# Kernel tuning notes

Measured on AMD Instinct MI355X. Metric: run time of the kernel, lower is better.

Reference implementation:

```python
import jax, jax.numpy as jnp
import numpy as np
import math

B, S, MEM, D, H = 2, 2048, 512, 1024, 16
DH = D // H  # 64


def setup_inputs() -> dict:
    key = jax.random.key(0)
    ks = jax.random.split(key, 12)
    s = 1.0 / math.sqrt(D)
    return {
        "x": jax.random.normal(ks[0], (B, S, D), jnp.float32),
        "mems": jax.random.normal(ks[1], (B, MEM, D), jnp.float32),
        "freqs_cis": jax.random.normal(ks[2], (S, 32), jnp.float32),
        "mask": jax.random.randint(ks[3], (B, MEM + S), 0, 2, jnp.int32),
        "Wq": jax.random.normal(ks[4], (D, D), jnp.float32) * s,
        "bq": jnp.zeros((D,), jnp.float32),
        "Wk": jax.random.normal(ks[5], (D, D), jnp.float32) * s,
        "bk": jnp.zeros((D,), jnp.float32),
        "Wv": jax.random.normal(ks[6], (D, D), jnp.float32) * s,
        "bv": jnp.zeros((D,), jnp.float32),
        "Wo": jax.random.normal(ks[7], (D, D), jnp.float32) * s,
        "bo": jnp.zeros((D,), jnp.float32),
    }


def _split_heads(t):
    # [B, T, D] -> [B, H, T, DH]
    b, t_, _ = t.shape
    return t.reshape(b, t_, H, DH).transpose(0, 2, 1, 3)


def reference(x, mems, freqs_cis, mask, Wq, bq, Wk, bk, Wv, bv, Wo, bo):
    # mems prepended along sequence for K/V (torch: c = cat([mems, x], 1))
    c = jnp.concatenate([mems, x], axis=1)  # [B, MEM+S, D]
    Q = _split_heads(x @ Wq.T + bq)          # [B, H, S, DH]
    K = _split_heads(c @ Wk.T + bk)          # [B, H, Skv, DH]
    V = _split_heads(c @ Wv.T + bv)          # [B, H, Skv, DH]

    scores = jnp.einsum("bhqd,bhkd->bhqk", Q, K) / math.sqrt(DH)
    m = mask.astype(jnp.float32)             # [B, Skv]
    scores = scores - 1e6 * (1.0 - m[:, None, None, :])
    attn = jax.nn.softmax(scores, axis=-1)   # dropout omitted (eval mode)
    out = jnp.einsum("bhqk,bhkd->bhqd", attn, V)  # [B, H, S, DH]
    out = out.transpose(0, 2, 1, 3).reshape(B, S, D)
    return out @ Wo.T + bo
```

## Files before the change

kernel.cpp:

```cpp
#include <hip/hip_runtime.h>
#include <math.h>

#define NB   2
#define SQ   2048
#define SMEM 512
#define SKVN 2560
#define ND   1024
#define NH   16
#define DHN  64

typedef unsigned short u16;
typedef short bf16x8 __attribute__((ext_vector_type(8)));
typedef float f32x4 __attribute__((ext_vector_type(4)));
typedef u16 u16x4 __attribute__((ext_vector_type(4)));
typedef u16 u16x8 __attribute__((ext_vector_type(8)));

#define CSC   0.1803368801111204f

__device__ __forceinline__ u16 f2bf(float f) {
    unsigned u = __float_as_uint(f);
    u += 0x7FFFu + ((u >> 16) & 1u);
    return (u16)(u >> 16);
}

__device__ __forceinline__ void async16(u16* lds, const u16* g) {
    __builtin_amdgcn_global_load_lds(
        (const __attribute__((address_space(1))) void*)g,
        (__attribute__((address_space(3))) void*)lds, 16, 0, 0);
}

__device__ __forceinline__ unsigned lds_off(const void* p) {
    return (unsigned)(uintptr_t)(const __attribute__((address_space(3))) void*)p;
}

__device__ __forceinline__ u16x4 tr_read(unsigned a) {
    u16x4 d;
    asm volatile("ds_read_b64_tr_b16 %0, %1" : "=v"(d) : "v"(a) : "memory");
    return d;
}

__device__ __forceinline__ unsigned cvtpk(float lo, float hi) {
    unsigned r;
    asm("v_cvt_pk_bf16_f32 %0, %1, %2" : "=v"(r) : "v"(lo), "v"(hi));
    return r;
}

__device__ __forceinline__ float exp2r(float x) {
    float r;
    asm("v_exp_f32 %0, %1" : "=v"(r) : "v"(x));
    return r;
}

union PKU { unsigned u[2]; u16x4 v; };
union U8  { struct { u16x4 lo, hi; } p; bf16x8 v; };

__global__ __launch_bounds__(256)
void cvt_all(const float* __restrict__ x, const float* __restrict__ mems,
             const float* __restrict__ W0, const float* __restrict__ W1,
             const float* __restrict__ W2, const float* __restrict__ W3,
             u16* __restrict__ xb, u16* __restrict__ memb,
             u16* __restrict__ d0, u16* __restrict__ d1,
             u16* __restrict__ d2, u16* __restrict__ d3,
             const int* __restrict__ mask, float* __restrict__ mbias)
{
    const int bid = blockIdx.x;
    if (bid >= 4608) {
        const int i = (bid - 4608) * 256 + threadIdx.x;
        if (i < NB * SKVN) mbias[i] = mask[i] ? 0.f : 1.0e6f * CSC;
        return;
    }
    size_t i = ((size_t)bid * 256 + threadIdx.x) * 8;
    const float* s; u16* d;
    if (i < 4194304) { s = x; d = xb; }
    else if (i < 5242880) { s = mems; d = memb; i -= 4194304; }
    else {
        size_t off = i - 5242880;
        const int wi = (int)(off >> 20);
        i = off & 1048575;
        switch (wi) {
            case 0:  s = W0; d = d0; break;
            case 1:  s = W1; d = d1; break;
            case 2:  s = W2; d = d2; break;
            default: s = W3; d = d3; break;
        }
    }
    float4 a = *(const float4*)(s + i);
    float4 b = *(const float4*)(s + i + 4);
    u16x8 o;
    o[0]=f2bf(a.x); o[1]=f2bf(a.y); o[2]=f2bf(a.z); o[3]=f2bf(a.w);
    o[4]=f2bf(b.x); o[5]=f2bf(b.y); o[6]=f2bf(b.z); o[7]=f2bf(b.w);
    *(u16x8*)(d + i) = o;
}

__device__ __forceinline__ const u16* arow_ptr(const u16* x, const u16* mems,
                                               int grow, int T, int memLen) {
    int b = grow >= T ? 1 : 0;
    int t = grow - b * T;
    if (memLen > 0 && t < memLen)
        return mems + ((size_t)(b * memLen + t)) * ND;
    return x + ((size_t)(b * (T - memLen) + (t - memLen))) * ND;
}

__device__ __forceinline__
void gemm_body(const u16* __restrict__ x, const u16* __restrict__ mems,
               const u16* __restrict__ W, const float* __restrict__ bias,
               void* __restrict__ out, int T, int memLen, int mode,
               int bx, int by, u16* As0, u16* As1, u16* Bs0, u16* Bs1)
{
    u16* As[2] = {As0, As1};
    u16* Bs[2] = {Bs0, Bs1};

    const int tid  = threadIdx.x;
    const int wave = tid >> 6, lane = tid & 63;
    const int lg = lane >> 4, li = lane & 15;
    const int wr = (wave >> 1) * 64, wc = (wave & 1) * 64;
    const int row0 = bx * 128, col0 = by * 128;

    const int srow = lane >> 2;
    const int sslot = lane & 3;

    f32x4 acc[4][4];
    const f32x4 zf = {0.f, 0.f, 0.f, 0.f};
#pragma unroll
    for (int m = 0; m < 4; ++m)
#pragma unroll
        for (int n = 0; n < 4; ++n) acc[m][n] = zf;

    auto stage = [&](int c, int kt) {
        const int k0 = kt * 32;
#pragma unroll
        for (int ch = wave; ch < 8; ch += 4) {
            const int r = ch * 16 + srow;
            const int gs = sslot ^ ((r ^ (r >> 2)) & 3);
            async16(&As[c][ch * 512],
                    arow_ptr(x, mems, row0 + r, T, memLen) + k0 + gs * 8);
        }
#pragma unroll
        for (int ch = wave; ch < 8; ch += 4) {
            const int r = ch * 16 + srow;
            const int gs = sslot ^ ((r ^ (r >> 2)) & 3);
            async16(&Bs[c][ch * 512],
                    W + (size_t)(col0 + r) * ND + k0 + gs * 8);
        }
    };

    stage(0, 0);
    int cur = 0;
    for (int kt = 0; kt < 32; ++kt) {
        __syncthreads();
        if (kt + 1 < 32) stage(cur ^ 1, kt + 1);

        bf16x8 af[4], bfr[4];
#pragma unroll
        for (int m = 0; m < 4; ++m) {
            const int r = wr + m * 16 + li;
            af[m] = *(const bf16x8*)&As[cur][r * 32 + ((lg ^ ((r ^ (r >> 2)) & 3)) << 3)];
        }
#pragma unroll
        for (int n = 0; n < 4; ++n) {
            const int r = wc + n * 16 + li;
            bfr[n] = *(const bf16x8*)&Bs[cur][r * 32 + ((lg ^ ((r ^ (r >> 2)) & 3)) << 3)];
        }
#pragma unroll
        for (int m = 0; m < 4; ++m)
#pragma unroll
            for (int n = 0; n < 4; ++n)
                acc[m][n] = __builtin_amdgcn_mfma_f32_16x16x32_bf16(
                                af[m], bfr[n], acc[m][n], 0, 0, 0);
        cur ^= 1;
    }

#pragma unroll
    for (int n = 0; n < 4; ++n) {
        const int col = col0 + wc + n * 16 + li;
        const float bv = bias[col];
#pragma unroll
        for (int m = 0; m < 4; ++m) {
            const int rbase = row0 + wr + m * 16 + 4 * lg;
            if (mode == 0) {
                float* o = (float*)out;
#pragma unroll
                for (int r = 0; r < 4; ++r)
                    o[(size_t)(rbase + r) * ND + col] = acc[m][n][r] + bv;
            } else if (mode == 1) {
                u16* o = (u16*)out;
                const int h = col >> 6, dh = col & 63;
#pragma unroll
                for (int r = 0; r < 4; ++r) {
                    const int grow = rbase + r;
                    const int b = grow >= T ? 1 : 0;
                    const int t = grow - b * T;
                    o[(((size_t)b * NH + h) * T + t) * DHN + dh] =
                        f2bf(acc[m][n][r] + bv);
                }
            } else {
                u16* o = (u16*)out;
                const int h = col >> 6, dh = col & 63;
                const int b = rbase >= T ? 1 : 0;
                const int t = rbase - b * T;
                u16x4 pk;
                pk[0] = f2bf(acc[m][n][0] + bv);
                pk[1] = f2bf(acc[m][n][1] + bv);
                pk[2] = f2bf(acc[m][n][2] + bv);
                pk[3] = f2bf(acc[m][n][3] + bv);
                *(u16x4*)&o[(((size_t)b * NH + h) * DHN + dh) * (size_t)T + t] = pk;
            }
        }
    }
}

__global__ __launch_bounds__(256)
void gemm_single(const u16* __restrict__ x, const u16* __restrict__ W,
                 const float* __restrict__ bias, void* __restrict__ out,
                 int T, int mode)
{
    __shared__ u16 As[2][128 * 32];
    __shared__ u16 Bs[2][128 * 32];
    gemm_body(x, nullptr, W, bias, out, T, 0, mode, blockIdx.x, blockIdx.y,
              As[0], As[1], Bs[0], Bs[1]);
}

__global__ __launch_bounds__(256)
void gemm_qkv(const u16* __restrict__ xb, const u16* __restrict__ memb,
              const u16* __restrict__ Wq, const float* __restrict__ bq, u16* Qb,
              const u16* __restrict__ Wk, const float* __restrict__ bk, u16* Kb,
              const u16* __restrict__ Wv, const float* __restrict__ bv, u16* Vtb)
{
    __shared__ u16 As[2][128 * 32];
    __shared__ u16 Bs[2][128 * 32];
    const int id = (blockIdx.x & 7) * 112 + (blockIdx.x >> 3);
    if (id < 256) {
        gemm_body(xb, nullptr, Wq, bq, Qb, SQ, 0, 1, id & 31, id >> 5,
                  As[0], As[1], Bs[0], Bs[1]);
    } else if (id < 576) {
        const int t = id - 256;
        gemm_body(xb, memb, Wk, bk, Kb, SKVN, SMEM, 1, t % 40, t / 40,
                  As[0], As[1], Bs[0], Bs[1]);
    } else {
        const int t = id - 576;
        gemm_body(xb, memb, Wv, bv, Vtb, SKVN, SMEM, 2, t % 40, t / 40,
                  As[0], As[1], Bs[0], Bs[1]);
    }
}

__global__ __launch_bounds__(256)
void attn_mfma(const u16* __restrict__ Qw, const u16* __restrict__ Kw,
               const u16* __restrict__ Vt, const float* __restrict__ mbias,
               u16* __restrict__ AO)
{
    __shared__ u16 Ks[2][64 * 64];
    __shared__ u16 Vs[2][64 * 64];
    __shared__ u16 Ps[4][2048];

    const int tid  = threadIdx.x;
    const int wave = tid >> 6, lane = tid & 63;
    const int lg = lane >> 4, li = lane & 15;

    const int wg = blockIdx.x;
    const int sw = (wg & 7) * 64 + (wg >> 3);
    const int bh = sw >> 4;
    const int q0 = (sw & 15) * 128;
    const int b = bh >> 4, h = bh & 15;

    const u16* Kg = Kw + (size_t)bh * SKVN * DHN;
    const u16* Vg = Vt + (size_t)bh * DHN * SKVN;
    const float* mrow = mbias + (size_t)b * SKVN;

    bf16x8 qA0, qA1, qB0, qB1;
    {
        const u16* Qp = Qw + ((size_t)bh * SQ + q0 + wave * 32 + li) * DHN;
        qA0 = *(const bf16x8*)(Qp + lg * 8);
        qA1 = *(const bf16x8*)(Qp + 32 + lg * 8);
        qB0 = *(const bf16x8*)(Qp + 16 * DHN + lg * 8);
        qB1 = *(const bf16x8*)(Qp + 16 * DHN + 32 + lg * 8);
    }

    U8 ou;
#pragma unroll
    for (int i = 0; i < 4; ++i) { ou.p.lo[i] = 0x3F80; ou.p.hi[i] = 0x3F80; }
    const bf16x8 onesb = ou.v;

    const int srow = lane >> 3, sslot = lane & 7;

    auto stage = [&](int c, int t) {
        const int kv0 = t * 64;
#pragma unroll
        for (int ch = wave; ch < 8; ch += 4) {
            const int r = ch * 8 + srow;
            async16(&Ks[c][ch * 512],
                    Kg + (size_t)(kv0 + r) * DHN + ((sslot ^ (r & 7)) << 3));
        }
#pragma unroll
        for (int ch = wave; ch < 8; ch += 4) {
            const int r = ch * 8 + srow;
            async16(&Vs[c][ch * 512],
                    Vg + (size_t)r * SKVN + kv0 + ((sslot ^ (r & 7)) << 3));
        }
    };

    f32x4 oA[4], oB[4], laccA, laccB;
    const f32x4 zf = {0.f, 0.f, 0.f, 0.f};
#pragma unroll
    for (int n = 0; n < 4; ++n) { oA[n] = zf; oB[n] = zf; }
    laccA = zf; laccB = zf;

    u16* Pw = &Ps[wave][0];
    const unsigned paA = lds_off(Pw) + 256u * lg + 8u * li;
    const unsigned paB = paA + 2048u;

    float mbn[4];
#pragma unroll
    for (int n = 0; n < 4; ++n) mbn[n] = mrow[n * 16 + li];

    stage(0, 0);
    int cur = 0;
    for (int t = 0; t < SKVN / 64; ++t) {
        float mbc[4];
#pragma unroll
        for (int n = 0; n < 4; ++n) mbc[n] = mbn[n];

        __syncthreads();
        if (t + 1 < SKVN / 64) {
            stage(cur ^ 1, t + 1);
#pragma unroll
            for (int n = 0; n < 4; ++n)
                mbn[n] = mrow[(t + 1) * 64 + n * 16 + li];
        }

        __builtin_amdgcn_s_setprio(1);
        f32x4 sA[4], sB[4];
#pragma unroll
        for (int n = 0; n < 4; ++n) {
            const int r = n * 16 + li;
            bf16x8 kb0 = *(const bf16x8*)&Ks[cur][r * 64 + ((lg ^ (r & 7)) << 3)];
            bf16x8 kb1 = *(const bf16x8*)&Ks[cur][r * 64 + (((4 + lg) ^ (r & 7)) << 3)];
            f32x4 z = zf;
            z     = __builtin_amdgcn_mfma_f32_16x16x32_bf16(qA0, kb0, z, 0, 0, 0);
            sA[n] = __builtin_amdgcn_mfma_f32_16x16x32_bf16(qA1, kb1, z, 0, 0, 0);
            f32x4 y = zf;
            y     = __builtin_amdgcn_mfma_f32_16x16x32_bf16(qB0, kb0, y, 0, 0, 0);
            sB[n] = __builtin_amdgcn_mfma_f32_16x16x32_bf16(qB1, kb1, y, 0, 0, 0);
        }
        __builtin_amdgcn_s_setprio(0);

#pragma unroll
        for (int n = 0; n < 4; ++n) {
            const float mb = mbc[n];
            const int pw = (n * 16 + li) * 16 + lg * 4;
            PKU ua;
            ua.u[0] = cvtpk(exp2r(fmaf(sA[n][0], CSC, -mb)),
                            exp2r(fmaf(sA[n][1], CSC, -mb)));
            ua.u[1] = cvtpk(exp2r(fmaf(sA[n][2], CSC, -mb)),
                            exp2r(fmaf(sA[n][3], CSC, -mb)));
            *(u16x4*)&Pw[pw] = ua.v;
            PKU ub;
            ub.u[0] = cvtpk(exp2r(fmaf(sB[n][0], CSC, -mb)),
                            exp2r(fmaf(sB[n][1], CSC, -mb)));
            ub.u[1] = cvtpk(exp2r(fmaf(sB[n][2], CSC, -mb)),
                            exp2r(fmaf(sB[n][3], CSC, -mb)));
            *(u16x4*)&Pw[1024 + pw] = ub.v;
        }

        u16x4 a00 = tr_read(paA);
        u16x4 a01 = tr_read(paA + 128);
        u16x4 a10 = tr_read(paA + 1024);
        u16x4 a11 = tr_read(paA + 1024 + 128);
        u16x4 b00 = tr_read(paB);
        u16x4 b01 = tr_read(paB + 128);
        u16x4 b10 = tr_read(paB + 1024);
        u16x4 b11 = tr_read(paB + 1024 + 128);
        asm volatile("s_waitcnt lgkmcnt(0)" ::: "memory");
        __builtin_amdgcn_sched_barrier(0);
        U8 pA0, pA1, pB0, pB1;
        pA0.p.lo = a00; pA0.p.hi = a01;
        pA1.p.lo = a10; pA1.p.hi = a11;
        pB0.p.lo = b00; pB0.p.hi = b01;
        pB1.p.lo = b10; pB1.p.hi = b11;

        __builtin_amdgcn_s_setprio(1);
        laccA = __builtin_amdgcn_mfma_f32_16x16x32_bf16(pA0.v, onesb, laccA, 0, 0, 0);
        laccA = __builtin_amdgcn_mfma_f32_16x16x32_bf16(pA1.v, onesb, laccA, 0, 0, 0);
        laccB = __builtin_amdgcn_mfma_f32_16x16x32_bf16(pB0.v, onesb, laccB, 0, 0, 0);
        laccB = __builtin_amdgcn_mfma_f32_16x16x32_bf16(pB1.v, onesb, laccB, 0, 0, 0);
#pragma unroll
        for (int n = 0; n < 4; ++n) {
            const int r = n * 16 + li;
            bf16x8 vb0 = *(const bf16x8*)&Vs[cur][r * 64 + ((lg ^ (r & 7)) << 3)];
            bf16x8 vb1 = *(const bf16x8*)&Vs[cur][r * 64 + (((4 + lg) ^ (r & 7)) << 3)];
            oA[n] = __builtin_amdgcn_mfma_f32_16x16x32_bf16(pA0.v, vb0, oA[n], 0, 0, 0);
            oA[n] = __builtin_amdgcn_mfma_f32_16x16x32_bf16(pA1.v, vb1, oA[n], 0, 0, 0);
            oB[n] = __builtin_amdgcn_mfma_f32_16x16x32_bf16(pB0.v, vb0, oB[n], 0, 0, 0);
            oB[n] = __builtin_amdgcn_mfma_f32_16x16x32_bf16(pB1.v, vb1, oB[n], 0, 0, 0);
        }
        __builtin_amdgcn_s_setprio(0);
        cur ^= 1;
    }

#pragma unroll
    for (int r = 0; r < 4; ++r) {
        const float invA = 1.f / laccA[r];
        const float invB = 1.f / laccB[r];
        const int rowA = q0 + wave * 32 + 4 * lg + r;
#pragma unroll
        for (int n = 0; n < 4; ++n) {
            const int col = h * DHN + n * 16 + li;
            AO[((size_t)b * SQ + rowA) * ND + col] = f2bf(oA[n][r] * invA);
            AO[((size_t)b * SQ + rowA + 16) * ND + col] = f2bf(oB[n][r] * invB);
        }
    }
}

extern "C" void kernel_launch(void* const* d_in, const int* in_sizes, int n_in,
                              void* d_out, int out_size, void* d_ws, size_t ws_size,
                              hipStream_t stream)
{
    const float* x    = (const float*)d_in[0];
    const float* mems = (const float*)d_in[1];
    const int*   mask = (const int*)d_in[3];
    const float* Wq = (const float*)d_in[4];  const float* bq = (const float*)d_in[5];
    const float* Wk = (const float*)d_in[6];  const float* bk = (const float*)d_in[7];
    const float* Wv = (const float*)d_in[8];  const float* bv = (const float*)d_in[9];
    const float* Wo = (const float*)d_in[10]; const float* bo = (const float*)d_in[11];
    float* out = (float*)d_out;

    u16* ws = (u16*)d_ws;
    u16* xb   = ws;
    u16* memb = xb   + (size_t)NB * SQ * ND;
    u16* Wqb  = memb + (size_t)NB * SMEM * ND;
    u16* Wkb  = Wqb + (size_t)ND * ND;
    u16* Wvb  = Wkb + (size_t)ND * ND;
    u16* Wob  = Wvb + (size_t)ND * ND;
    u16* Qb   = Wob + (size_t)ND * ND;
    u16* Kb   = Qb  + (size_t)NB * NH * SQ * DHN;
    u16* Vtb  = Kb  + (size_t)NB * NH * SKVN * DHN;
    u16* AOb  = Vtb + (size_t)NB * NH * SKVN * DHN;
    float* mbias = (float*)(AOb + (size_t)NB * SQ * ND);

    const dim3 blk(256);
    cvt_all<<<dim3(4628), blk, 0, stream>>>(x, mems, Wq, Wk, Wv, Wo,
                                            xb, memb, Wqb, Wkb, Wvb, Wob,
                                            mask, mbias);
    gemm_qkv<<<dim3(896), blk, 0, stream>>>(xb, memb,
                                            Wqb, bq, Qb,
                                            Wkb, bk, Kb,
                                            Wvb, bv, Vtb);
    attn_mfma<<<dim3(512), blk, 0, stream>>>(Qb, Kb, Vtb, mbias, AOb);
    gemm_single<<<dim3(32, 8), blk, 0, stream>>>(AOb, Wob, bo, (void*)out, SQ, 0);
}
```

Before: 172.8 us.

## Split attention KV range in two halves and add combine kernel

Result: slower. 177.5 us (+2.7%).

```diff
diff --git a/kernel.cpp b/kernel.cpp
--- a/kernel.cpp
+++ b/kernel.cpp
@@ -8,6 +8,7 @@
 #define ND   1024
 #define NH   16
 #define DHN  64
+#define NBH  32
 
 typedef unsigned short u16;
 typedef short bf16x8 __attribute__((ext_vector_type(8)));
@@ -21,6 +22,10 @@
     unsigned u = __float_as_uint(f);
     u += 0x7FFFu + ((u >> 16) & 1u);
     return (u16)(u >> 16);
+}
+
+__device__ __forceinline__ float bf2f(u16 v) {
+    return __uint_as_float(((unsigned)v) << 16);
 }
 
 __device__ __forceinline__ void async16(u16* lds, const u16* g) {
@@ -246,7 +251,7 @@
 __global__ __launch_bounds__(256)
 void attn_mfma(const u16* __restrict__ Qw, const u16* __restrict__ Kw,
                const u16* __restrict__ Vt, const float* __restrict__ mbias,
-               u16* __restrict__ AO)
+               u16* __restrict__ PO, float* __restrict__ Lb)
 {
     __shared__ u16 Ks[2][64 * 64];
     __shared__ u16 Vs[2][64 * 64];
@@ -257,14 +262,15 @@
     const int lg = lane >> 4, li = lane & 15;
 
     const int wg = blockIdx.x;
-    const int sw = (wg & 7) * 64 + (wg >> 3);
-    const int bh = sw >> 4;
-    const int q0 = (sw & 15) * 128;
-    const int b = bh >> 4, h = bh & 15;
+    const int sw = (wg & 7) * 128 + (wg >> 3);
+    const int bh   = sw >> 5;
+    const int q0   = ((sw >> 1) & 15) * 128;
+    const int half = sw & 1;
+    const int t0 = half * 20, t1 = t0 + 20;
 
     const u16* Kg = Kw + (size_t)bh * SKVN * DHN;
     const u16* Vg = Vt + (size_t)bh * DHN * SKVN;
-    const float* mrow = mbias + (size_t)b * SKVN;
+    const float* mrow = mbias + (size_t)(bh >> 4) * SKVN;
 
     bf16x8 qA0, qA1, qB0, qB1;
     {
@@ -310,17 +316,17 @@
 
     float mbn[4];
 #pragma unroll
-    for (int n = 0; n < 4; ++n) mbn[n] = mrow[n * 16 + li];
-
-    stage(0, 0);
+    for (int n = 0; n < 4; ++n) mbn[n] = mrow[t0 * 64 + n * 16 + li];
+
+    stage(0, t0);
     int cur = 0;
-    for (int t = 0; t < SKVN / 64; ++t) {
+    for (int t = t0; t < t1; ++t) {
         float mbc[4];
 #pragma unroll
         for (int n = 0; n < 4; ++n) mbc[n] = mbn[n];
 
         __syncthreads();
-        if (t + 1 < SKVN / 64) {
+        if (t + 1 < t1) {
             stage(cur ^ 1, t + 1);
 #pragma unroll
             for (int n = 0; n < 4; ++n)
@@ -396,18 +402,46 @@
         cur ^= 1;
     }
 
+    u16* POh = PO + (size_t)half * NBH * SQ * DHN;
+    float* Lh = Lb + (size_t)half * NBH * SQ;
 #pragma unroll
     for (int r = 0; r < 4; ++r) {
-        const float invA = 1.f / laccA[r];
-        const float invB = 1.f / laccB[r];
         const int rowA = q0 + wave * 32 + 4 * lg + r;
 #pragma unroll
         for (int n = 0; n < 4; ++n) {
-            const int col = h * DHN + n * 16 + li;
-            AO[((size_t)b * SQ + rowA) * ND + col] = f2bf(oA[n][r] * invA);
-            AO[((size_t)b * SQ + rowA + 16) * ND + col] = f2bf(oB[n][r] * invB);
-        }
-    }
+            const int c = n * 16 + li;
+            POh[((size_t)bh * SQ + rowA) * DHN + c] = f2bf(oA[n][r]);
+            POh[((size_t)bh * SQ + rowA + 16) * DHN + c] = f2bf(oB[n][r]);
+        }
+        if (li == 0) {
+            Lh[(size_t)bh * SQ + rowA] = laccA[r];
+            Lh[(size_t)bh * SQ + rowA + 16] = laccB[r];
+        }
+    }
+}
+
+__global__ __launch_bounds__(256)
+void attn_combine(const u16* __restrict__ PO, const float* __restrict__ Lb,
+                  u16* __restrict__ AO)
+{
+    const size_t idx = ((size_t)blockIdx.x * 256 + threadIdx.x) * 8;
+    const int row = (int)(idx >> 10);
+    const int col = (int)(idx & 1023);
+    const int b = row >> 11, q = row & 2047;
+    const int h = col >> 6, dh = col & 63;
+    const int bh = b * NH + h;
+    const size_t pbase = ((size_t)bh * SQ + q) * DHN + dh;
+    const size_t hs = (size_t)NBH * SQ * DHN;
+
+    u16x8 pa = *(const u16x8*)&PO[pbase];
+    u16x8 pb = *(const u16x8*)&PO[hs + pbase];
+    const float l = Lb[(size_t)bh * SQ + q] + Lb[(size_t)NBH * SQ + bh * SQ + q];
+    const float inv = 1.f / l;
+    u16x8 o;
+#pragma unroll
+    for (int i = 0; i < 8; ++i)
+        o[i] = f2bf((bf2f(pa[i]) + bf2f(pb[i])) * inv);
+    *(u16x8*)&AO[idx] = o;
 }
 
 extern "C" void kernel_launch(void* const* d_in, const int* in_sizes, int n_in,
@@ -435,6 +469,8 @@
     u16* Vtb  = Kb  + (size_t)NB * NH * SKVN * DHN;
     u16* AOb  = Vtb + (size_t)NB * NH * SKVN * DHN;
     float* mbias = (float*)(AOb + (size_t)NB * SQ * ND);
+    u16* POb  = (u16*)(mbias + NB * SKVN);
+    float* Lbf = (float*)(POb + (size_t)2 * NBH * SQ * DHN);
 
     const dim3 blk(256);
     cvt_all<<<dim3(4628), blk, 0, stream>>>(x, mems, Wq, Wk, Wv, Wo,
@@ -444,6 +480,7 @@
                                             Wqb, bq, Qb,
                                             Wkb, bk, Kb,
                                             Wvb, bv, Vtb);
-    attn_mfma<<<dim3(512), blk, 0, stream>>>(Qb, Kb, Vtb, mbias, AOb);
+    attn_mfma<<<dim3(1024), blk, 0, stream>>>(Qb, Kb, Vtb, mbias, POb, Lbf);
+    attn_combine<<<dim3(2048), blk, 0, stream>>>(POb, Lbf, AOb);
     gemm_single<<<dim3(32, 8), blk, 0, stream>>>(AOb, Wob, bo, (void*)out, SQ, 0);
 }
```
